# Optimization experiments

Measured on AMD Instinct MI355X. Metric: run time of the kernel, lower is better.

Reference implementation:

```python
import jax, jax.numpy as jnp
import numpy as np
import math

B = 128
STRIDES = (8.0, 16.0, 32.0)
GRIDS = (128, 64, 32)
C_Q = 4
LAMBDA_BBOX = 5.0
LAMBDA_QUALITY = 0.05
FOCAL_ALPHA = 0.25
FOCAL_GAMMA = 2.0
EPS = 1e-6


def setup_inputs() -> dict:
    key = jax.random.key(0)
    ks = jax.random.split(key, 12)
    inp = {}
    for i, (hw, name) in enumerate(zip(GRIDS, ('det_map8', 'det_map16', 'det_map32'))):
        inp[name] = jax.random.normal(ks[i], (B, 5, hw, hw), dtype=jnp.float32)
    for i, (hw, name) in enumerate(zip(GRIDS, ('qual_map8', 'qual_map16', 'qual_map32'))):
        inp[name] = jax.random.normal(ks[3 + i], (B, C_Q, hw, hw), dtype=jnp.float32)
    # realistic GT boxes inside a 1024x1024 image; every 16th sample invalid (x1 < 0)
    x1 = jax.random.uniform(ks[6], (B,), minval=0.0, maxval=600.0)
    y1 = jax.random.uniform(ks[7], (B,), minval=0.0, maxval=600.0)
    w = jax.random.uniform(ks[8], (B,), minval=64.0, maxval=320.0)
    h = jax.random.uniform(ks[9], (B,), minval=64.0, maxval=320.0)
    boxes = jnp.stack([x1, y1, jnp.minimum(x1 + w, 1023.0), jnp.minimum(y1 + h, 1023.0)], axis=1)
    invalid = (jnp.arange(B) % 16) == 0
    boxes = jnp.where(invalid[:, None], -1.0, boxes)
    inp['gt_bboxes'] = boxes.astype(jnp.float32)
    inp['gt_quality'] = jax.random.uniform(ks[10], (B, C_Q), dtype=jnp.float32)
    return inp


def _level_losses(det, qual, stride, gt_bboxes, gt_quality, valid):
    Bn, _, H, W = det.shape
    gy, gx = jnp.meshgrid(jnp.arange(H, dtype=jnp.float32),
                          jnp.arange(W, dtype=jnp.float32), indexing='ij')
    cx = (gx + 0.5) * stride  # [H,W]
    cy = (gy + 0.5) * stride
    x1 = gt_bboxes[:, 0, None, None]
    y1 = gt_bboxes[:, 1, None, None]
    x2 = gt_bboxes[:, 2, None, None]
    y2 = gt_bboxes[:, 3, None, None]
    in_box = (cx > x1) & (cx < x2) & (cy > y1) & (cy < y2) & valid[:, None, None]  # [B,H,W]

    # --- focal loss on conf channel ---
    z = det[:, 0]
    t = in_box.astype(jnp.float32)
    ce = jnp.maximum(z, 0.0) - z * t + jnp.log1p(jnp.exp(-jnp.abs(z)))
    p = jax.nn.sigmoid(z)
    pt = jnp.where(t == 1, p, 1.0 - p)
    a_t = jnp.where(t == 1, FOCAL_ALPHA, 1.0 - FOCAL_ALPHA)
    focal = a_t * (1.0 - pt) ** FOCAL_GAMMA * ce
    conf = (focal * valid[:, None, None].astype(jnp.float32)).mean()

    # --- CIoU on positive cells (vectorized, masked) ---
    pl = jnp.exp(jnp.clip(det[:, 1], -6.0, 6.0)) * stride
    pt_ = jnp.exp(jnp.clip(det[:, 2], -6.0, 6.0)) * stride
    pr = jnp.exp(jnp.clip(det[:, 3], -6.0, 6.0)) * stride
    pb = jnp.exp(jnp.clip(det[:, 4], -6.0, 6.0)) * stride
    # safe GT distances: positive dummy outside the mask to avoid NaN poisoning
    gl = jnp.where(in_box, cx - x1, 1.0)
    gtl = jnp.where(in_box, cy - y1, 1.0)
    gr = jnp.where(in_box, x2 - cx, 1.0)
    gb = jnp.where(in_box, y2 - cy, 1.0)
    pw = pl + pr
    ph = pt_ + pb
    gw = gl + gr
    gh = gtl + gb
    iw = jnp.clip(jnp.minimum(pl, gl) + jnp.minimum(pr, gr), 0.0)
    ih = jnp.clip(jnp.minimum(pt_, gtl) + jnp.minimum(pb, gb), 0.0)
    inter = iw * ih
    union = pw * ph + gw * gh - inter + EPS
    iou = inter / union
    c_w = jnp.maximum(pl, gl) + jnp.maximum(pr, gr)
    c_h = jnp.maximum(pt_, gtl) + jnp.maximum(pb, gb)
    c2 = c_w ** 2 + c_h ** 2 + EPS
    dcx = (pr - pl) / 2.0 - (gr - gl) / 2.0
    dcy = (pb - pt_) / 2.0 - (gb - gtl) / 2.0
    rho2 = dcx ** 2 + dcy ** 2
    v = (4.0 / math.pi ** 2) * (jnp.arctan(gw / (gh + EPS)) - jnp.arctan(pw / (ph + EPS))) ** 2
    alpha_v = jax.lax.stop_gradient(v / (1.0 - iou + v + EPS))
    ciou = 1.0 - iou + rho2 / c2 + alpha_v * v  # [B,H,W]
    npos_b = in_box.sum(axis=(1, 2))  # [B]
    ciou_mean = (ciou * t).sum(axis=(1, 2)) / jnp.maximum(npos_b, 1).astype(jnp.float32)
    has_pos = npos_b > 0
    bbox = jnp.where(has_pos, ciou_mean, 0.0).sum()

    # --- quality BCE at the positive cell closest to box center ---
    bcx = (gt_bboxes[:, 0] + gt_bboxes[:, 2]) / 2.0
    bcy = (gt_bboxes[:, 1] + gt_bboxes[:, 3]) / 2.0
    dist2 = (cx - bcx[:, None, None]) ** 2 + (cy - bcy[:, None, None]) ** 2
    dist2 = jnp.where(in_box, dist2, jnp.inf)
    idx = jnp.argmin(dist2.reshape(Bn, -1), axis=1)  # [B]
    qual_flat = qual.reshape(Bn, qual.shape[1], -1)  # [B,Cq,HW]
    best = jnp.take_along_axis(qual_flat, idx[:, None, None], axis=2)[:, :, 0]  # [B,Cq]
    q_tgt = jnp.clip(gt_quality, 0.05, 0.95)
    bce = -(q_tgt * jax.nn.log_sigmoid(best) + (1.0 - q_tgt) * jax.nn.log_sigmoid(-best))
    qual_loss = jnp.where(has_pos, bce.mean(axis=1), 0.0).sum()

    return conf, bbox, qual_loss, has_pos.sum()


def _stage_a_loss(det_maps, qual_maps, gt_bboxes, gt_quality):
    valid = gt_bboxes[:, 0] >= 0
    total_conf = jnp.float32(0.0)
    total_bbox = jnp.float32(0.0)
    total_qual = jnp.float32(0.0)
    n_pos = jnp.int32(0)
    for det, qual, stride in zip(det_maps, qual_maps, STRIDES):
        c, b_, q, n = _level_losses(det, qual, stride, gt_bboxes, gt_quality, valid)
        total_conf = total_conf + c
        total_bbox = total_bbox + b_
        total_qual = total_qual + q
        n_pos = n_pos + n
    denom = jnp.maximum(n_pos, 1).astype(jnp.float32)
    total_bbox = jnp.where(n_pos > 0, total_bbox / denom, total_bbox)
    total_qual = jnp.where(n_pos > 0, total_qual / denom, total_qual)
    total = total_conf + LAMBDA_BBOX * total_bbox + LAMBDA_QUALITY * total_qual
    return total, total_conf, total_bbox, total_qual


def reference(det_map8, det_map16, det_map32, qual_map8, qual_map16, qual_map32,
              gt_bboxes, gt_quality):
    return _stage_a_loss((det_map8, det_map16, det_map32),
                         (qual_map8, qual_map16, qual_map32),
                         gt_bboxes, gt_quality)
```

## Files before the change

### kernel.cpp

```cpp
#include <hip/hip_runtime.h>
#include <math.h>


#define NBLK 384

__device__ __forceinline__ float rcpf(float x) { return __builtin_amdgcn_rcpf(x); }

__device__ __forceinline__ float logsigf(float x) {
    return fminf(x, 0.f) - __logf(1.f + __expf(-fabsf(x)));
}

__device__ __forceinline__ void ciou_one(
    float cx, float cy, float stride, float ls, float ts, float rs, float bs,
    float x1, float y1, float x2, float y2, float bcx, float bcy, int locj,
    float& ciou, int& np, unsigned long long& pk)
{
    const float pl  = __expf(fminf(fmaxf(ls, -6.f), 6.f)) * stride;
    const float pt_ = __expf(fminf(fmaxf(ts, -6.f), 6.f)) * stride;
    const float pr  = __expf(fminf(fmaxf(rs, -6.f), 6.f)) * stride;
    const float pb  = __expf(fminf(fmaxf(bs, -6.f), 6.f)) * stride;
    const float gl  = cx - x1, gtl = cy - y1, gr = x2 - cx, gb = y2 - cy;
    const float pw = pl + pr, ph = pt_ + pb;
    const float gw = gl + gr, gh = gtl + gb;
    const float iw = fmaxf(fminf(pl, gl) + fminf(pr, gr), 0.f);
    const float ih = fmaxf(fminf(pt_, gtl) + fminf(pb, gb), 0.f);
    const float inter = iw * ih;
    const float uni   = pw * ph + gw * gh - inter + 1e-6f;
    const float iou   = inter * rcpf(uni);
    const float cw_ = fmaxf(pl, gl) + fmaxf(pr, gr);
    const float ch_ = fmaxf(pt_, gtl) + fmaxf(pb, gb);
    const float c2  = cw_ * cw_ + ch_ * ch_ + 1e-6f;
    const float dcx = 0.5f * (pr - pl) - 0.5f * (gr - gl);
    const float dcy = 0.5f * (pb - pt_) - 0.5f * (gb - gtl);
    const float rho2 = dcx * dcx + dcy * dcy;
    const float dv = atanf(gw * rcpf(gh + 1e-6f)) - atanf(pw * rcpf(ph + 1e-6f));
    const float v  = (4.f / (float)(M_PI * M_PI)) * dv * dv;
    const float alpha = v * rcpf(1.f - iou + v + 1e-6f);
    ciou += 1.f - iou + rho2 * rcpf(c2) + alpha * v;
    ++np;
    const float ddx = cx - bcx, ddy = cy - bcy;
    const float dist2 = ddx * ddx + ddy * ddy;
    const unsigned long long cand =
        ((unsigned long long)__float_as_uint(dist2) << 32) | (unsigned)locj;
    pk = cand < pk ? cand : pk;
}

__device__ __forceinline__ void focal4(const float4& d0, const bool inb[4], float& conf)
{
    const float zs[4] = { d0.x, d0.y, d0.z, d0.w };
    #pragma unroll
    for (int j = 0; j < 4; ++j) {
        const float z  = zs[j];
        const float e  = __expf(-fabsf(z));
        const float ce = fmaxf(z, 0.f) - (inb[j] ? z : 0.f) + __logf(1.f + e);
        const float inv = rcpf(1.f + e);
        const float p  = (z >= 0.f) ? inv : e * inv;
        const float pt = inb[j] ? p : 1.f - p;
        const float at = inb[j] ? 0.25f : 0.75f;
        const float om = 1.f - pt;
        conf += at * om * om * ce;
    }
}

__device__ __forceinline__ void stripe4(
    const float* __restrict__ det, size_t c0base, int loc, size_t HW, float stride,
    const float cxs[4], const bool cxok[4], float cy,
    float x1, float y1, float x2, float y2, float bcx, float bcy,
    const float4& d0, float& conf, float& ciou, int& np, unsigned long long& pk)
{
    const bool cyok = (cy > y1) & (cy < y2);
    bool inb[4]; bool anyb = false;
    #pragma unroll
    for (int j = 0; j < 4; ++j) { inb[j] = cxok[j] & cyok; anyb |= inb[j]; }
    focal4(d0, inb, conf);
    if (__any(anyb)) {
        const float4 d1 = *(const float4*)(det + c0base + HW + (size_t)loc);
        const float4 d2 = *(const float4*)(det + c0base + 2 * HW + (size_t)loc);
        const float4 d3 = *(const float4*)(det + c0base + 3 * HW + (size_t)loc);
        const float4 d4 = *(const float4*)(det + c0base + 4 * HW + (size_t)loc);
        const float ls[4] = { d1.x, d1.y, d1.z, d1.w };
        const float ts[4] = { d2.x, d2.y, d2.z, d2.w };
        const float rs[4] = { d3.x, d3.y, d3.z, d3.w };
        const float bs[4] = { d4.x, d4.y, d4.z, d4.w };
        #pragma unroll
        for (int j = 0; j < 4; ++j)
            if (inb[j])
                ciou_one(cxs[j], cy, stride, ls[j], ts[j], rs[j], bs[j],
                         x1, y1, x2, y2, bcx, bcy, loc + j, ciou, np, pk);
    }
}

__global__ __launch_bounds__(1024) void level_k(
    const float* __restrict__ det8, const float* __restrict__ det16, const float* __restrict__ det32,
    const float* __restrict__ q8, const float* __restrict__ q16, const float* __restrict__ q32,
    const float* __restrict__ gtb, const float* __restrict__ gtq,
    float4* __restrict__ contrib)
{
    const int tid = (int)threadIdx.x;
    const int bid = (int)blockIdx.x;

    int b, log2W, l2q, nstripe;
    const float* det; const float* q; float stride; float inv_denom; size_t HW;
    bool active = true;
    if (bid < 128) {
        b = bid; det = det8; q = q8;
        stride = 8.f;  log2W = 7; HW = 16384; l2q = 14; nstripe = 4; inv_denom = 1.f / 2097152.f;
    } else if (bid < 256) {
        b = bid - 128; det = det16; q = q16;
        stride = 16.f; log2W = 6; HW = 4096;  l2q = 12; nstripe = 1; inv_denom = 1.f / 524288.f;
    } else {
        b = bid - 256; det = det32; q = q32;
        stride = 32.f; log2W = 5; HW = 1024;  l2q = 10; nstripe = 1; inv_denom = 1.f / 131072.f;
        active = (tid < 256);
    }

    float conf = 0.f, ciou = 0.f; int np = 0;
    unsigned long long pk = ~0ULL;

    const float x1 = gtb[b * 4 + 0];
    if (x1 >= 0.f && active) {
        const float y1 = gtb[b * 4 + 1];
        const float x2 = gtb[b * 4 + 2];
        const float y2 = gtb[b * 4 + 3];
        const float bcx = 0.5f * (x1 + x2);
        const float bcy = 0.5f * (y1 + y2);
        const size_t c0base = (size_t)(b * 5) * HW;
        const int Wm1 = (1 << log2W) - 1;
        const int loc0 = tid << 2;

        const int xi = loc0 & Wm1;
        float cxs[4]; bool cxok[4];
        #pragma unroll
        for (int j = 0; j < 4; ++j) {
            cxs[j]  = ((float)(xi + j) + 0.5f) * stride;
            cxok[j] = (cxs[j] > x1) & (cxs[j] < x2);
        }
        float cy = ((float)(loc0 >> log2W) + 0.5f) * stride;

        if (nstripe == 4) {
            const float dcy = stride * (float)(4096 >> log2W);
            float4 d[4];
            #pragma unroll
            for (int s = 0; s < 4; ++s)
                d[s] = *(const float4*)(det + c0base + (size_t)(loc0 + s * 4096));
            #pragma unroll
            for (int s = 0; s < 4; ++s) {
                stripe4(det, c0base, loc0 + s * 4096, HW, stride, cxs, cxok, cy,
                        x1, y1, x2, y2, bcx, bcy, d[s], conf, ciou, np, pk);
                cy += dcy;
            }
        } else {
            const float4 d0 = *(const float4*)(det + c0base + (size_t)loc0);
            stripe4(det, c0base, loc0, HW, stride, cxs, cxok, cy,
                    x1, y1, x2, y2, bcx, bcy, d0, conf, ciou, np, pk);
        }
        conf *= inv_denom;
    }

    #pragma unroll
    for (int off = 32; off > 0; off >>= 1) {
        conf += __shfl_down(conf, off);
        ciou += __shfl_down(ciou, off);
        np   += __shfl_down(np, off);
        unsigned long long o = __shfl_down(pk, off);
        pk = o < pk ? o : pk;
    }

    __shared__ float s_conf[16], s_ciou[16];
    __shared__ int   s_np[16];
    __shared__ unsigned long long s_pk[16];
    const int wid = tid >> 6;
    if ((tid & 63) == 0) {
        s_conf[wid] = conf; s_ciou[wid] = ciou; s_np[wid] = np; s_pk[wid] = pk;
    }
    __syncthreads();
    if (tid == 0) {
        float cf = 0.f, ci = 0.f; int nt = 0;
        unsigned long long mn = ~0ULL;
        #pragma unroll
        for (int w = 0; w < 16; ++w) {
            cf += s_conf[w]; ci += s_ciou[w]; nt += s_np[w];
            mn = s_pk[w] < mn ? s_pk[w] : mn;
        }
        float bbv = 0.f, qlv = 0.f, flag = 0.f;
        if (nt > 0) {
            bbv = ci * rcpf((float)nt);
            const unsigned idx = (unsigned)(mn & 0xffffffffULL);
            float s = 0.f;
            #pragma unroll
            for (int c = 0; c < 4; ++c) {
                const float best = q[((size_t)(b * 4 + c) << l2q) + idx];
                const float qt = fminf(fmaxf(gtq[b * 4 + c], 0.05f), 0.95f);
                s -= qt * logsigf(best) + (1.f - qt) * logsigf(-best);
            }
            qlv = 0.25f * s;
            flag = 1.f;
        }
        contrib[bid] = make_float4(cf, bbv, qlv, flag);
    }
}

__global__ __launch_bounds__(512) void fin_k(
    const float4* __restrict__ contrib, float* __restrict__ out)
{
    const int i = threadIdx.x;
    float cf = 0.f, bb = 0.f, ql = 0.f, nf = 0.f;
    if (i < NBLK) {
        const float4 v = contrib[i];
        cf = v.x; bb = v.y; ql = v.z; nf = v.w;
    }
    #pragma unroll
    for (int off = 32; off > 0; off >>= 1) {
        cf += __shfl_down(cf, off);
        bb += __shfl_down(bb, off);
        ql += __shfl_down(ql, off);
        nf += __shfl_down(nf, off);
    }
    __shared__ float wc[8], wb[8], wq[8], wn[8];
    if ((i & 63) == 0) { wc[i >> 6] = cf; wb[i >> 6] = bb; wq[i >> 6] = ql; wn[i >> 6] = nf; }
    __syncthreads();
    if (i == 0) {
        float conf_t = 0.f, tb0 = 0.f, tq0 = 0.f, nsum = 0.f;
        #pragma unroll
        for (int w = 0; w < 8; ++w) { conf_t += wc[w]; tb0 += wb[w]; tq0 += wq[w]; nsum += wn[w]; }
        const int ntot = (int)(nsum + 0.5f);
        const float denom = fmaxf((float)ntot, 1.f);
        const float tb = (ntot > 0) ? tb0 / denom : tb0;
        const float tq = (ntot > 0) ? tq0 / denom : tq0;
        out[0] = conf_t + 5.f * tb + 0.05f * tq;
        out[1] = conf_t;
        out[2] = tb;
        out[3] = tq;
    }
}

extern "C" void kernel_launch(void* const* d_in, const int* in_sizes, int n_in,
                              void* d_out, int out_size, void* d_ws, size_t ws_size,
                              hipStream_t stream) {
    const float* det8  = (const float*)d_in[0];
    const float* det16 = (const float*)d_in[1];
    const float* det32 = (const float*)d_in[2];
    const float* q8    = (const float*)d_in[3];
    const float* q16   = (const float*)d_in[4];
    const float* q32   = (const float*)d_in[5];
    const float* gtb   = (const float*)d_in[6];
    const float* gtq   = (const float*)d_in[7];
    float* out = (float*)d_out;

    float4* contrib = (float4*)d_ws;

    hipLaunchKernelGGL(level_k, dim3(NBLK), dim3(1024), 0, stream,
                       det8, det16, det32, q8, q16, q32, gtb, gtq, contrib);
    hipLaunchKernelGGL(fin_k, dim3(1), dim3(512), 0, stream,
                       contrib, out);
}
```

Baseline: 18.19 us.

## Split stride-8 level across two blocks per sample and finish its quality loss in fin_k

Each stride-8 sample is now handled by two blocks, each covering half the map, so the launch grows to 512 blocks and the per-block serial work shrinks. Because each half only sees part of the map, its partial CIoU, positive count and packed nearest-index go to workspace. fin_k then merges the halves and evaluates the quality BCE for stride 8. The focal term is also reformulated as sigmoid-squared times softplus, and the bbox-channel loads are issued before the focal math to overlap latency. The cost is extra workspace traffic and more serial work in the single-block finish kernel.

```diff
diff --git a/kernel.cpp b/kernel.cpp
--- a/kernel.cpp
+++ b/kernel.cpp
@@ -2,7 +2,7 @@
 #include <math.h>
 
 
-#define NBLK 384
+#define NBLK 512
 
 __device__ __forceinline__ float rcpf(float x) { return __builtin_amdgcn_rcpf(x); }
 
@@ -50,15 +50,15 @@
     const float zs[4] = { d0.x, d0.y, d0.z, d0.w };
     #pragma unroll
     for (int j = 0; j < 4; ++j) {
-        const float z  = zs[j];
-        const float e  = __expf(-fabsf(z));
-        const float ce = fmaxf(z, 0.f) - (inb[j] ? z : 0.f) + __logf(1.f + e);
-        const float inv = rcpf(1.f + e);
-        const float p  = (z >= 0.f) ? inv : e * inv;
-        const float pt = inb[j] ? p : 1.f - p;
-        const float at = inb[j] ? 0.25f : 0.75f;
-        const float om = 1.f - pt;
-        conf += at * om * om * ce;
+        const float u   = inb[j] ? -zs[j] : zs[j];
+        const float e   = __expf(-fabsf(u));
+        const float ope = 1.f + e;
+        const float L   = __logf(ope);
+        const float inv = rcpf(ope);
+        const float sg  = (u >= 0.f) ? inv : e * inv;
+        const float sp  = fmaxf(u, 0.f) + L;
+        const float at  = inb[j] ? 0.25f : 0.75f;
+        conf += at * sg * sg * sp;
     }
 }
 
@@ -72,12 +72,19 @@
     bool inb[4]; bool anyb = false;
     #pragma unroll
     for (int j = 0; j < 4; ++j) { inb[j] = cxok[j] & cyok; anyb |= inb[j]; }
+    const bool wa = __any(anyb);
+
+    float4 d1, d2, d3, d4;
+    if (wa) {
+        d1 = *(const float4*)(det + c0base + HW + (size_t)loc);
+        d2 = *(const float4*)(det + c0base + 2 * HW + (size_t)loc);
+        d3 = *(const float4*)(det + c0base + 3 * HW + (size_t)loc);
+        d4 = *(const float4*)(det + c0base + 4 * HW + (size_t)loc);
+    }
+
     focal4(d0, inb, conf);
-    if (__any(anyb)) {
-        const float4 d1 = *(const float4*)(det + c0base + HW + (size_t)loc);
-        const float4 d2 = *(const float4*)(det + c0base + 2 * HW + (size_t)loc);
-        const float4 d3 = *(const float4*)(det + c0base + 3 * HW + (size_t)loc);
-        const float4 d4 = *(const float4*)(det + c0base + 4 * HW + (size_t)loc);
+
+    if (wa) {
         const float ls[4] = { d1.x, d1.y, d1.z, d1.w };
         const float ts[4] = { d2.x, d2.y, d2.z, d2.w };
         const float rs[4] = { d3.x, d3.y, d3.z, d3.w };
@@ -92,27 +99,30 @@
 
 __global__ __launch_bounds__(1024) void level_k(
     const float* __restrict__ det8, const float* __restrict__ det16, const float* __restrict__ det32,
-    const float* __restrict__ q8, const float* __restrict__ q16, const float* __restrict__ q32,
+    const float* __restrict__ q16, const float* __restrict__ q32,
     const float* __restrict__ gtb, const float* __restrict__ gtq,
-    float4* __restrict__ contrib)
+    float4* __restrict__ contrib,
+    unsigned long long* __restrict__ pk_p, float* __restrict__ ciou_p, int* __restrict__ np_p)
 {
     const int tid = (int)threadIdx.x;
     const int bid = (int)blockIdx.x;
 
-    int b, log2W, l2q, nstripe;
+    int b, base, log2W, l2q, nstripe;
     const float* det; const float* q; float stride; float inv_denom; size_t HW;
-    bool active = true;
-    if (bid < 128) {
-        b = bid; det = det8; q = q8;
-        stride = 8.f;  log2W = 7; HW = 16384; l2q = 14; nstripe = 4; inv_denom = 1.f / 2097152.f;
-    } else if (bid < 256) {
-        b = bid - 128; det = det16; q = q16;
+    bool active = true, owner = false;
+    if (bid < 256) {
+        b = bid >> 1; base = (bid & 1) * 8192; det = det8; q = nullptr;
+        stride = 8.f;  log2W = 7; HW = 16384; l2q = 14; nstripe = 2; inv_denom = 1.f / 2097152.f;
+    } else if (bid < 384) {
+        b = bid - 256; base = 0; det = det16; q = q16; owner = true;
         stride = 16.f; log2W = 6; HW = 4096;  l2q = 12; nstripe = 1; inv_denom = 1.f / 524288.f;
     } else {
-        b = bid - 256; det = det32; q = q32;
+        b = bid - 384; base = 0; det = det32; q = q32; owner = true;
         stride = 32.f; log2W = 5; HW = 1024;  l2q = 10; nstripe = 1; inv_denom = 1.f / 131072.f;
         active = (tid < 256);
     }
+
+    const float4 gq = owner ? *(const float4*)(gtq + b * 4) : make_float4(0, 0, 0, 0);
 
     float conf = 0.f, ciou = 0.f; int np = 0;
     unsigned long long pk = ~0ULL;
@@ -126,7 +136,7 @@
         const float bcy = 0.5f * (y1 + y2);
         const size_t c0base = (size_t)(b * 5) * HW;
         const int Wm1 = (1 << log2W) - 1;
-        const int loc0 = tid << 2;
+        const int loc0 = base + (tid << 2);
 
         const int xi = loc0 & Wm1;
         float cxs[4]; bool cxok[4];
@@ -137,18 +147,14 @@
         }
         float cy = ((float)(loc0 >> log2W) + 0.5f) * stride;
 
-        if (nstripe == 4) {
+        if (nstripe == 2) {
             const float dcy = stride * (float)(4096 >> log2W);
-            float4 d[4];
-            #pragma unroll
-            for (int s = 0; s < 4; ++s)
-                d[s] = *(const float4*)(det + c0base + (size_t)(loc0 + s * 4096));
-            #pragma unroll
-            for (int s = 0; s < 4; ++s) {
-                stripe4(det, c0base, loc0 + s * 4096, HW, stride, cxs, cxok, cy,
-                        x1, y1, x2, y2, bcx, bcy, d[s], conf, ciou, np, pk);
-                cy += dcy;
-            }
+            const float4 dA = *(const float4*)(det + c0base + (size_t)loc0);
+            const float4 dB = *(const float4*)(det + c0base + (size_t)(loc0 + 4096));
+            stripe4(det, c0base, loc0, HW, stride, cxs, cxok, cy,
+                    x1, y1, x2, y2, bcx, bcy, dA, conf, ciou, np, pk);
+            stripe4(det, c0base, loc0 + 4096, HW, stride, cxs, cxok, cy + dcy,
+                    x1, y1, x2, y2, bcx, bcy, dB, conf, ciou, np, pk);
         } else {
             const float4 d0 = *(const float4*)(det + c0base + (size_t)loc0);
             stripe4(det, c0base, loc0, HW, stride, cxs, cxok, cy,
@@ -182,33 +188,73 @@
             cf += s_conf[w]; ci += s_ciou[w]; nt += s_np[w];
             mn = s_pk[w] < mn ? s_pk[w] : mn;
         }
-        float bbv = 0.f, qlv = 0.f, flag = 0.f;
-        if (nt > 0) {
-            bbv = ci * rcpf((float)nt);
-            const unsigned idx = (unsigned)(mn & 0xffffffffULL);
-            float s = 0.f;
-            #pragma unroll
-            for (int c = 0; c < 4; ++c) {
-                const float best = q[((size_t)(b * 4 + c) << l2q) + idx];
-                const float qt = fminf(fmaxf(gtq[b * 4 + c], 0.05f), 0.95f);
-                s -= qt * logsigf(best) + (1.f - qt) * logsigf(-best);
+        if (!owner) {
+            pk_p[bid] = mn; ciou_p[bid] = ci; np_p[bid] = nt;
+            contrib[bid] = make_float4(cf, 0.f, 0.f, 0.f);
+        } else {
+            float bbv = 0.f, qlv = 0.f, flag = 0.f;
+            if (nt > 0) {
+                bbv = ci * rcpf((float)nt);
+                const unsigned idx = (unsigned)(mn & 0xffffffffULL);
+                const float gqs[4] = { gq.x, gq.y, gq.z, gq.w };
+                float s = 0.f;
+                #pragma unroll
+                for (int c = 0; c < 4; ++c) {
+                    const float best = q[((size_t)(b * 4 + c) << l2q) + idx];
+                    const float qt = fminf(fmaxf(gqs[c], 0.05f), 0.95f);
+                    s -= qt * logsigf(best) + (1.f - qt) * logsigf(-best);
+                }
+                qlv = 0.25f * s;
+                flag = 1.f;
             }
-            qlv = 0.25f * s;
-            flag = 1.f;
-        }
-        contrib[bid] = make_float4(cf, bbv, qlv, flag);
+            contrib[bid] = make_float4(cf, bbv, qlv, flag);
+        }
     }
 }
 
 __global__ __launch_bounds__(512) void fin_k(
-    const float4* __restrict__ contrib, float* __restrict__ out)
+    const float* __restrict__ q8, const float* __restrict__ gtq,
+    const float4* __restrict__ contrib,
+    const unsigned long long* __restrict__ pk_p, const float* __restrict__ ciou_p,
+    const int* __restrict__ np_p,
+    float* __restrict__ out)
 {
     const int i = threadIdx.x;
-    float cf = 0.f, bb = 0.f, ql = 0.f, nf = 0.f;
-    if (i < NBLK) {
-        const float4 v = contrib[i];
-        cf = v.x; bb = v.y; ql = v.z; nf = v.w;
-    }
+    __shared__ unsigned sidx[128];
+
+    const float4 v = contrib[i];
+    float cf = v.x, bb = v.y, ql = v.z, nf = v.w;
+
+    if (i < 128) {
+        const float ci = ciou_p[2 * i] + ciou_p[2 * i + 1];
+        const int   np = np_p[2 * i] + np_p[2 * i + 1];
+        unsigned long long mn = pk_p[2 * i];
+        const unsigned long long p1 = pk_p[2 * i + 1];
+        mn = p1 < mn ? p1 : mn;
+        if (np > 0) {
+            bb += ci * rcpf((float)np);
+            nf += 1.f;
+            sidx[i] = (unsigned)(mn & 0xffffffffULL);
+        } else {
+            sidx[i] = 0xFFFFFFFFu;
+        }
+    }
+    __syncthreads();
+
+    {
+        const int s = i >> 2, c = i & 3;
+        const unsigned idx = sidx[s];
+        float term = 0.f;
+        if (idx != 0xFFFFFFFFu) {
+            const float best = q8[((size_t)(s * 4 + c) << 14) + idx];
+            const float qt = fminf(fmaxf(gtq[s * 4 + c], 0.05f), 0.95f);
+            term = -(qt * logsigf(best) + (1.f - qt) * logsigf(-best));
+        }
+        term += __shfl_down(term, 2);
+        term += __shfl_down(term, 1);
+        if (c == 0) ql += 0.25f * term;
+    }
+
     #pragma unroll
     for (int off = 32; off > 0; off >>= 1) {
         cf += __shfl_down(cf, off);
@@ -248,9 +294,13 @@
     float* out = (float*)d_out;
 
     float4* contrib = (float4*)d_ws;
+    unsigned long long* pk_p = (unsigned long long*)((char*)d_ws + 8192);
+    float* ciou_p = (float*)((char*)d_ws + 10240);
+    int*   np_p   = (int*)((char*)d_ws + 11264);
 
     hipLaunchKernelGGL(level_k, dim3(NBLK), dim3(1024), 0, stream,
-                       det8, det16, det32, q8, q16, q32, gtb, gtq, contrib);
+                       det8, det16, det32, q16, q32, gtb, gtq,
+                       contrib, pk_p, ciou_p, np_p);
     hipLaunchKernelGGL(fin_k, dim3(1), dim3(512), 0, stream,
-                       contrib, out);
-}
+                       q8, gtq, contrib, pk_p, ciou_p, np_p, out);
+}
```

Measured after the change: 19.38 us. +6.5%, slower.
